# Optimization experiments

Measured on AMD Instinct MI355X. Metric: run time of the kernel, lower is better.

The kernel has to match this reference:

```python
import jax, jax.numpy as jnp
import numpy as np
import math

B, IN, OUT = 1024, 512, 512


def setup_inputs() -> dict:
    key = jax.random.key(0)
    ks = jax.random.split(key, 7)
    std = 1.0 / math.sqrt(IN)
    x = jax.random.normal(ks[0], (B, IN), dtype=jnp.float32)
    base_weight = jax.random.uniform(ks[1], (OUT, IN), dtype=jnp.float32, minval=-std, maxval=std)
    chirplet_weights = jax.random.uniform(ks[2], (OUT, IN), dtype=jnp.float32, minval=-std, maxval=std)
    # scale init ones, frequency ones, translation zeros; add small jitter for a non-degenerate test point
    scale = 1.0 + 0.1 * jax.random.normal(ks[3], (OUT, IN), dtype=jnp.float32)
    translation = 0.1 * jax.random.normal(ks[4], (OUT, IN), dtype=jnp.float32)
    frequency = 1.0 + 0.1 * jax.random.normal(ks[5], (OUT, IN), dtype=jnp.float32)
    bias = jax.random.uniform(ks[6], (OUT,), dtype=jnp.float32, minval=-std, maxval=std)
    return {"x": x, "base_weight": base_weight, "chirplet_weights": chirplet_weights,
            "scale": scale, "translation": translation, "frequency": frequency, "bias": bias}


def reference(x, base_weight, chirplet_weights, scale, translation, frequency, bias):
    TWO_PI = 2.0 * math.pi
    # base linear path: SiLU(x) @ W^T
    base_out = jnp.einsum('bi,oi->bo', jax.nn.silu(x), base_weight)
    # chirplet path: (b, o, i) intermediate reduced over i
    x_scaled = (x[:, None, :] - translation[None, :, :]) / scale[None, :, :]  # (B, OUT, IN)
    chirplet = jnp.cos(TWO_PI * frequency[None, :, :] * x_scaled) * jnp.exp(-0.5 * x_scaled ** 2)
    chirplet_out = jnp.einsum('boi,oi->bo', chirplet, chirplet_weights)
    return base_out + chirplet_out + bias[None, :]
```

## Files before the change

### kernel.cpp

```cpp
#include <hip/hip_runtime.h>
#include <hip/hip_bf16.h>

#define B_ 1024
#define IN_ 512
#define OUT_ 512
#define BTILE 64
#define OTILE 32
#define ITILE 8
#define KSPLIT 16
#define KCHUNK (IN_ / KSPLIT)
#define NCHUNKS (KCHUNK / ITILE)
#define P4STRIDE 128
#define P2STRIDE 64
#define XSTRIDE 68

typedef float v2f __attribute__((ext_vector_type(2)));
#define PKFMA(a, b, c) __builtin_elementwise_fma((v2f)(a), (v2f)(b), (v2f)(c))

__device__ __forceinline__ float fast_exp2(float x) {
#if __has_builtin(__builtin_amdgcn_exp2f)
    return __builtin_amdgcn_exp2f(x);
#else
    return __exp2f(x);
#endif
}
__device__ __forceinline__ float fast_log2(float x) {
#if __has_builtin(__builtin_amdgcn_logf)
    return __builtin_amdgcn_logf(x);
#else
    return __log2f(x);
#endif
}
__device__ __forceinline__ float fast_cos_rev(float x) {
#if __has_builtin(__builtin_amdgcn_cosf)
    return __builtin_amdgcn_cosf(x);
#else
    return __cosf(x * 6.2831853071795864f);
#endif
}
__device__ __forceinline__ float fast_rcp(float x) {
#if __has_builtin(__builtin_amdgcn_rcpf)
    return __builtin_amdgcn_rcpf(x);
#else
    return 1.0f / x;
#endif
}

__global__ __launch_bounds__(256, 8) void chirplet_kernel(
    const float* __restrict__ x,
    const float* __restrict__ W,
    const float* __restrict__ Wc,
    const float* __restrict__ S,
    const float* __restrict__ T,
    const float* __restrict__ F,
    const float* __restrict__ bias,
    float* __restrict__ out)
{
    __shared__ __align__(16) float p4_lds[ITILE * P4STRIDE];
    __shared__ __align__(16) float p2_lds[ITILE * P2STRIDE];
    __shared__ __align__(16) float x_lds[ITILE * XSTRIDE];
    __shared__ __align__(16) float s_lds[ITILE * XSTRIDE];

    const int tid = threadIdx.x;
    const int o0 = blockIdx.x * OTILE;
    const int b0 = blockIdx.y * BTILE;
    const int k0 = blockIdx.z * KCHUNK;

    const int oc = tid & 15;
    const int bq = tid >> 4;

    const int xrow = tid >> 2;
    const int xq   = tid & 3;

    const int pol = tid & 31;
    const int pi  = tid >> 5;

    const float LOG2E = 1.4426950408889634f;
    const float GK    = 0.8493218002880191f;

    v2f acc2[2][2] = {{{0.f,0.f},{0.f,0.f}},{{0.f,0.f},{0.f,0.f}}};

    for (int c = 0; c < NCHUNKS; ++c) {
        const int ib = k0 + c * ITILE;

        {
            const float2 v = *(const float2*)(x + (size_t)(b0 + xrow) * IN_ + ib + xq * 2);
            const float xf[2] = { v.x, v.y };
            #pragma unroll
            for (int j = 0; j < 2; ++j) {
                const int col = xq * 2 + j;
                float xv  = xf[j];
                float sig = fast_rcp(1.0f + fast_exp2(-xv * LOG2E));
                x_lds[col * XSTRIDE + xrow] = xv;
                s_lds[col * XSTRIDE + xrow] = xv * sig;
            }
        }

        {
            const size_t go = (size_t)(o0 + pol) * IN_ + ib + pi;
            const float s  = S[go];
            const float t  = T[go];
            const float f  = F[go];
            const float w  = W[go];
            const float wc = Wc[go];
            const float rs = fast_rcp(s);
            const float a  = f * rs;
            float4 p0; float2 p1;
            p0.x = a;
            p0.y = -a * t + (wc < 0.0f ? 0.5f : 0.0f);
            p0.z = rs * GK;
            p0.w = -t * rs * GK;
            p1.x = fast_log2(fabsf(wc));
            p1.y = w;
            *(float4*)&p4_lds[pi * P4STRIDE + pol * 4] = p0;
            *(float2*)&p2_lds[pi * P2STRIDE + pol * 2] = p1;
        }
        __syncthreads();

        #pragma unroll 4
        for (int i = 0; i < ITILE; ++i) {
            const float4 abcd[2] = {
                *(const float4*)&p4_lds[i * P4STRIDE + oc * 4],
                *(const float4*)&p4_lds[i * P4STRIDE + (oc + 16) * 4] };
            const float2 lww[2] = {
                *(const float2*)&p2_lds[i * P2STRIDE + oc * 2],
                *(const float2*)&p2_lds[i * P2STRIDE + (oc + 16) * 2] };
            const v2f* xp = (const v2f*)&x_lds[i * XSTRIDE + bq * 4];
            const v2f* sp = (const v2f*)&s_lds[i * XSTRIDE + bq * 4];
            const v2f xk2[2] = { xp[0], xp[1] };
            const v2f sk2[2] = { sp[0], sp[1] };
            #pragma unroll
            for (int o = 0; o < 2; ++o) {
                const v2f aa = { abcd[o].x, abcd[o].x };
                const v2f bb = { abcd[o].y, abcd[o].y };
                const v2f cc = { abcd[o].z, abcd[o].z };
                const v2f dd = { abcd[o].w, abcd[o].w };
                const v2f lw = { lww[o].x, lww[o].x };
                const v2f wv = { lww[o].y, lww[o].y };
                #pragma unroll
                for (int p = 0; p < 2; ++p) {
                    v2f rev = PKFMA(aa, xk2[p], bb);
                    v2f u   = PKFMA(cc, xk2[p], dd);
                    v2f arg = PKFMA(-u, u, lw);
                    v2f co, e;
                    co.x = fast_cos_rev(rev.x);
                    co.y = fast_cos_rev(rev.y);
                    e.x  = fast_exp2(arg.x);
                    e.y  = fast_exp2(arg.y);
                    acc2[o][p] = PKFMA(co, e, acc2[o][p]);
                    acc2[o][p] = PKFMA(sk2[p], wv, acc2[o][p]);
                }
            }
        }
        __syncthreads();
    }

    const float badd0 = (blockIdx.z == 0) ? bias[o0 + oc] : 0.0f;
    const float badd1 = (blockIdx.z == 0) ? bias[o0 + oc + 16] : 0.0f;
    const float badd[2] = { badd0, badd1 };
    #pragma unroll
    for (int o = 0; o < 2; ++o) {
        #pragma unroll
        for (int p = 0; p < 2; ++p) {
            #pragma unroll
            for (int j = 0; j < 2; ++j) {
                const int b = b0 + bq * 4 + p * 2 + j;
                float* dst = &out[(size_t)b * OUT_ + o0 + oc + o * 16];
                const float val = (j == 0 ? acc2[o][p].x : acc2[o][p].y) + badd[o];
#if defined(__HIP_DEVICE_COMPILE__)
                unsafeAtomicAdd(dst, val);
#else
                atomicAdd(dst, val);
#endif
            }
        }
    }
}

extern "C" void kernel_launch(void* const* d_in, const int* in_sizes, int n_in,
                              void* d_out, int out_size, void* d_ws, size_t ws_size,
                              hipStream_t stream) {
    const float* x    = (const float*)d_in[0];
    const float* W    = (const float*)d_in[1];
    const float* Wc   = (const float*)d_in[2];
    const float* S    = (const float*)d_in[3];
    const float* T    = (const float*)d_in[4];
    const float* F    = (const float*)d_in[5];
    const float* bias = (const float*)d_in[6];
    float* out = (float*)d_out;

    hipMemsetAsync(out, 0, (size_t)out_size * sizeof(float), stream);

    dim3 grid(OUT_ / OTILE, B_ / BTILE, KSPLIT);
    chirplet_kernel<<<grid, 256, 0, stream>>>(x, W, Wc, S, T, F, bias, out);
}
```

Before: 128.9 us.

## Move SiLU base linear path onto bf16 MFMA instead of packed FMA

Removes the per-element SiLU(x)*W FMA from the inner chirplet loop and instead stages SiLU(x) and W as bf16 tiles in LDS across the whole K chunk. A single 16x16x32 bf16 MFMA per output sub-tile computes the base path at the end. This cuts VALU work and LDS traffic in the hot loop, at the cost of bf16 precision on the base path and relying on the MFMA output lane mapping matching the accumulator layout.

```diff
diff --git a/kernel.cpp b/kernel.cpp
--- a/kernel.cpp
+++ b/kernel.cpp
@@ -11,12 +11,20 @@
 #define KCHUNK (IN_ / KSPLIT)
 #define NCHUNKS (KCHUNK / ITILE)
 #define P4STRIDE 128
-#define P2STRIDE 64
+#define PLSTRIDE 32
 #define XSTRIDE 68
-
-typedef float v2f __attribute__((ext_vector_type(2)));
+#define ASTRIDE 40
+
+typedef float v2f   __attribute__((ext_vector_type(2)));
+typedef float f32x4 __attribute__((ext_vector_type(4)));
+typedef short s16x8 __attribute__((ext_vector_type(8)));
 #define PKFMA(a, b, c) __builtin_elementwise_fma((v2f)(a), (v2f)(b), (v2f)(c))
 
+__device__ __forceinline__ unsigned short f2bf(float f) {
+    union { float f; unsigned int u; } v; v.f = f;
+    unsigned int b = v.u + 0x7FFFu + ((v.u >> 16) & 1u);
+    return (unsigned short)(b >> 16);
+}
 __device__ __forceinline__ float fast_exp2(float x) {
 #if __has_builtin(__builtin_amdgcn_exp2f)
     return __builtin_amdgcn_exp2f(x);
@@ -57,11 +65,14 @@
     float* __restrict__ out)
 {
     __shared__ __align__(16) float p4_lds[ITILE * P4STRIDE];
-    __shared__ __align__(16) float p2_lds[ITILE * P2STRIDE];
+    __shared__ __align__(16) float plw_lds[ITILE * PLSTRIDE];
     __shared__ __align__(16) float x_lds[ITILE * XSTRIDE];
-    __shared__ __align__(16) float s_lds[ITILE * XSTRIDE];
-
-    const int tid = threadIdx.x;
+    __shared__ __align__(16) unsigned short sA_lds[BTILE * ASTRIDE];
+    __shared__ __align__(16) unsigned short wB_lds[OTILE * ASTRIDE];
+
+    const int tid  = threadIdx.x;
+    const int wave = tid >> 6;
+    const int lane = tid & 63;
     const int o0 = blockIdx.x * OTILE;
     const int b0 = blockIdx.y * BTILE;
     const int k0 = blockIdx.z * KCHUNK;
@@ -86,14 +97,16 @@
         {
             const float2 v = *(const float2*)(x + (size_t)(b0 + xrow) * IN_ + ib + xq * 2);
             const float xf[2] = { v.x, v.y };
+            unsigned int packed = 0;
             #pragma unroll
             for (int j = 0; j < 2; ++j) {
                 const int col = xq * 2 + j;
                 float xv  = xf[j];
                 float sig = fast_rcp(1.0f + fast_exp2(-xv * LOG2E));
                 x_lds[col * XSTRIDE + xrow] = xv;
-                s_lds[col * XSTRIDE + xrow] = xv * sig;
+                packed |= (unsigned int)f2bf(xv * sig) << (16 * j);
             }
+            *(unsigned int*)&sA_lds[xrow * ASTRIDE + c * 8 + xq * 2] = packed;
         }
 
         {
@@ -105,15 +118,14 @@
             const float wc = Wc[go];
             const float rs = fast_rcp(s);
             const float a  = f * rs;
-            float4 p0; float2 p1;
+            float4 p0;
             p0.x = a;
             p0.y = -a * t + (wc < 0.0f ? 0.5f : 0.0f);
             p0.z = rs * GK;
             p0.w = -t * rs * GK;
-            p1.x = fast_log2(fabsf(wc));
-            p1.y = w;
             *(float4*)&p4_lds[pi * P4STRIDE + pol * 4] = p0;
-            *(float2*)&p2_lds[pi * P2STRIDE + pol * 2] = p1;
+            plw_lds[pi * PLSTRIDE + pol] = fast_log2(fabsf(wc));
+            wB_lds[pol * ASTRIDE + c * 8 + pi] = f2bf(w);
         }
         __syncthreads();
 
@@ -122,51 +134,56 @@
             const float4 abcd[2] = {
                 *(const float4*)&p4_lds[i * P4STRIDE + oc * 4],
                 *(const float4*)&p4_lds[i * P4STRIDE + (oc + 16) * 4] };
-            const float2 lww[2] = {
-                *(const float2*)&p2_lds[i * P2STRIDE + oc * 2],
-                *(const float2*)&p2_lds[i * P2STRIDE + (oc + 16) * 2] };
+            const float lw[2] = {
+                plw_lds[i * PLSTRIDE + oc],
+                plw_lds[i * PLSTRIDE + oc + 16] };
             const v2f* xp = (const v2f*)&x_lds[i * XSTRIDE + bq * 4];
-            const v2f* sp = (const v2f*)&s_lds[i * XSTRIDE + bq * 4];
             const v2f xk2[2] = { xp[0], xp[1] };
-            const v2f sk2[2] = { sp[0], sp[1] };
             #pragma unroll
             for (int o = 0; o < 2; ++o) {
                 const v2f aa = { abcd[o].x, abcd[o].x };
                 const v2f bb = { abcd[o].y, abcd[o].y };
                 const v2f cc = { abcd[o].z, abcd[o].z };
                 const v2f dd = { abcd[o].w, abcd[o].w };
-                const v2f lw = { lww[o].x, lww[o].x };
-                const v2f wv = { lww[o].y, lww[o].y };
+                const v2f lwv = { lw[o], lw[o] };
                 #pragma unroll
                 for (int p = 0; p < 2; ++p) {
                     v2f rev = PKFMA(aa, xk2[p], bb);
                     v2f u   = PKFMA(cc, xk2[p], dd);
-                    v2f arg = PKFMA(-u, u, lw);
+                    v2f arg = PKFMA(-u, u, lwv);
                     v2f co, e;
                     co.x = fast_cos_rev(rev.x);
                     co.y = fast_cos_rev(rev.y);
                     e.x  = fast_exp2(arg.x);
                     e.y  = fast_exp2(arg.y);
                     acc2[o][p] = PKFMA(co, e, acc2[o][p]);
-                    acc2[o][p] = PKFMA(sk2[p], wv, acc2[o][p]);
                 }
             }
         }
         __syncthreads();
     }
 
-    const float badd0 = (blockIdx.z == 0) ? bias[o0 + oc] : 0.0f;
-    const float badd1 = (blockIdx.z == 0) ? bias[o0 + oc + 16] : 0.0f;
-    const float badd[2] = { badd0, badd1 };
+    const int q8 = (lane >> 4) * 8;
+    const s16x8 af  = *(const s16x8*)&sA_lds[(wave * 16 + (lane & 15)) * ASTRIDE + q8];
+    const s16x8 bf0 = *(const s16x8*)&wB_lds[(lane & 15) * ASTRIDE + q8];
+    const s16x8 bf1 = *(const s16x8*)&wB_lds[((lane & 15) + 16) * ASTRIDE + q8];
+    const f32x4 mz = { 0.f, 0.f, 0.f, 0.f };
+    const f32x4 m0 = __builtin_amdgcn_mfma_f32_16x16x32_bf16(af, bf0, mz, 0, 0, 0);
+    const f32x4 m1 = __builtin_amdgcn_mfma_f32_16x16x32_bf16(af, bf1, mz, 0, 0, 0);
+
+    const float badd[2] = { (blockIdx.z == 0) ? bias[o0 + oc] : 0.0f,
+                            (blockIdx.z == 0) ? bias[o0 + oc + 16] : 0.0f };
     #pragma unroll
     for (int o = 0; o < 2; ++o) {
         #pragma unroll
         for (int p = 0; p < 2; ++p) {
             #pragma unroll
             for (int j = 0; j < 2; ++j) {
-                const int b = b0 + bq * 4 + p * 2 + j;
+                const int reg = p * 2 + j;
+                const int b = b0 + bq * 4 + reg;
                 float* dst = &out[(size_t)b * OUT_ + o0 + oc + o * 16];
-                const float val = (j == 0 ? acc2[o][p].x : acc2[o][p].y) + badd[o];
+                const float mm = (o == 0) ? m0[reg] : m1[reg];
+                const float val = (j == 0 ? acc2[o][p].x : acc2[o][p].y) + mm + badd[o];
 #if defined(__HIP_DEVICE_COMPILE__)
                 unsafeAtomicAdd(dst, val);
 #else
```

New measurement: 125.2 us (median of 2 runs). 1.03x faster.
